# Performance work log

Hardware: AMD Instinct MI355X
Metric: run time of the kernel (lower is better)

Reference implementation:

```python
import jax, jax.numpy as jnp
import numpy as np

B, S, D, H, HD, L, V = 32, 512, 512, 8, 64, 6, 64000
EPS = 1e-5

def _layer_norm(x, g, b):
    mu = jnp.mean(x, axis=-1, keepdims=True)
    var = jnp.mean(jnp.square(x - mu), axis=-1, keepdims=True)
    return (x - mu) * jax.lax.rsqrt(var + EPS) * g + b

def _sinusoidal_pe():
    pos = np.arange(S)[:, None].astype(np.float32)
    div = np.exp(np.arange(0, D, 2).astype(np.float32) * -(np.log(10000.0) / D))
    pe = np.zeros((S, D), dtype=np.float32)
    pe[:, 0::2] = np.sin(pos * div)
    pe[:, 1::2] = np.cos(pos * div)
    return jnp.asarray(pe)

def setup_inputs() -> dict:
    key = jax.random.key(0)
    ks = jax.random.split(key, 8)
    std = 0.02
    return {
        'tokens': jax.random.randint(ks[0], (B, S), 0, V),
        'mask': jnp.ones((B, S), dtype=jnp.int32),
        'emb': jax.random.normal(ks[1], (V, D), jnp.float32) * std,
        'pe': _sinusoidal_pe(),
        'Wq': jax.random.normal(ks[2], (L, H, D, HD), jnp.float32) * std,
        'Wk': jax.random.normal(ks[3], (L, H, D, HD), jnp.float32) * std,
        'Wv': jax.random.normal(ks[4], (L, H, D, HD), jnp.float32) * std,
        'Wo': jax.random.normal(ks[5], (L, D, D), jnp.float32) * std,
        'ln1_g': jnp.ones((L, D), jnp.float32),
        'ln1_b': jnp.zeros((L, D), jnp.float32),
        'W1': jax.random.normal(ks[6], (L, D, 4 * D), jnp.float32) * std,
        'b1': jnp.zeros((L, 4 * D), jnp.float32),
        'W2': jax.random.normal(ks[7], (L, 4 * D, D), jnp.float32) * std,
        'b2': jnp.zeros((L, D), jnp.float32),
        'ln2_g': jnp.ones((L, D), jnp.float32),
        'ln2_b': jnp.zeros((L, D), jnp.float32),
    }

def reference(tokens, mask, emb, pe, Wq, Wk, Wv, Wo, ln1_g, ln1_b, W1, b1, W2, b2, ln2_g, ln2_b):
    # Eval mode: all dropouts are identity.
    x = emb[tokens] + pe[None, :S, :]               # [B,S,D]
    neg_inf = jnp.finfo(x.dtype).min
    mask_b = (mask == 0)[:, None, None, :]          # [B,1,1,S] broadcast over heads & queries
    scale = HD ** -0.5
    for l in range(L):
        q = jnp.einsum('bsd,hde->bhse', x, Wq[l])
        k = jnp.einsum('bsd,hde->bhse', x, Wk[l])
        v = jnp.einsum('bsd,hde->bhse', x, Wv[l])
        w = jnp.einsum('bhse,bhte->bhst', q, k) * scale
        w = jnp.where(mask_b, neg_inf, w)
        a = jax.nn.softmax(w, axis=-1)
        o = jnp.einsum('bhst,bhte->bhse', a, v)     # [B,H,S,HD]
        o = o.transpose(0, 2, 1, 3).reshape(x.shape[0], S, D)  # concat heads
        x = _layer_norm(x + o @ Wo[l], ln1_g[l], ln1_b[l])
        h = jax.nn.gelu(x @ W1[l] + b1[l], approximate=False) @ W2[l] + b2[l]
        x = _layer_norm(x + h, ln2_g[l], ln2_b[l])
    return x
```

## Files before the change

### kernel.cpp

```cpp
#include <hip/hip_runtime.h>

#define BB 32
#define SS 512
#define DD 512
#define HH 8
#define HDH 64
#define LL 6
#define DFF 2048
#define MM (BB*SS)

typedef __attribute__((ext_vector_type(4))) float f32x4;
typedef __attribute__((ext_vector_type(8))) short s16x8;
typedef __attribute__((ext_vector_type(4))) short s16x4;

__device__ __forceinline__ unsigned short f2bf(float f) {
    union { float f; unsigned u; } v; v.f = f;
    unsigned r = v.u + 0x7fffu + ((v.u >> 16) & 1u);
    return (unsigned short)(r >> 16);
}
__device__ __forceinline__ float bf2f(unsigned short b) {
    union { unsigned u; float f; } v; v.u = ((unsigned)b) << 16;
    return v.f;
}

__device__ __forceinline__ f32x4 mfma_bf16(s16x8 a, s16x8 b, f32x4 c) {
    asm("v_mfma_f32_16x16x32_bf16 %0, %1, %2, %0" : "+v"(c) : "v"(a), "v"(b));
    return c;
}

__device__ __forceinline__ void gload_lds16(const void* g, void* l) {
    __builtin_amdgcn_global_load_lds(
        (__attribute__((address_space(1))) void*)g,
        (__attribute__((address_space(3))) void*)l, 16, 0, 0);
}

__device__ __forceinline__ void tile_transpose_conv(
    const float* __restrict__ src, int srcPitch,
    unsigned short* __restrict__ dst, int dstPitch,
    float* lt)
{
    const int t = threadIdx.x;
    #pragma unroll
    for (int it = 0; it < 4; ++it) {
        int r = it * 16 + (t >> 4);
        int c = (t & 15) * 4;
        f32x4 v = *(const f32x4*)(src + (size_t)r * srcPitch + c);
        lt[r * 65 + c + 0] = v[0];
        lt[r * 65 + c + 1] = v[1];
        lt[r * 65 + c + 2] = v[2];
        lt[r * 65 + c + 3] = v[3];
    }
    __syncthreads();
    int nn = t >> 2;
    int kc = (t & 3) * 16;
    s16x8 o0, o1;
    #pragma unroll
    for (int i = 0; i < 8; ++i)  o0[i] = (short)f2bf(lt[(kc + i) * 65 + nn]);
    #pragma unroll
    for (int i = 0; i < 8; ++i)  o1[i] = (short)f2bf(lt[(kc + 8 + i) * 65 + nn]);
    *(s16x8*)(dst + (size_t)nn * dstPitch + kc) = o0;
    *(s16x8*)(dst + (size_t)nn * dstPitch + kc + 8) = o1;
}

__global__ __launch_bounds__(256) void k_tconv_qkv(const float* __restrict__ Wq,
                                                   const float* __restrict__ Wk,
                                                   const float* __restrict__ Wv,
                                                   unsigned short* __restrict__ dst) {
    __shared__ float lt[64 * 65];
    int bid = blockIdx.x;
    int which = bid / 384;
    int rem = bid - which * 384;
    int l = rem >> 6;
    int h = (rem >> 3) & 7;
    int kt = rem & 7;
    const float* W = which == 0 ? Wq : (which == 1 ? Wk : Wv);
    const float* srcT = W + (((size_t)(l * HH + h) * 512) + kt * 64) * 64;
    unsigned short* dstT = dst + ((size_t)l * 1536 + which * 512 + h * 64) * 512 + kt * 64;
    tile_transpose_conv(srcT, 64, dstT, 512, lt);
}

__global__ __launch_bounds__(256) void k_tconv_w(const float* __restrict__ src,
                                                 unsigned short* __restrict__ dst,
                                                 int K, int N) {
    __shared__ float lt[64 * 65];
    int tpb = (K >> 6) * (N >> 6);
    int bid = blockIdx.x;
    int l = bid / tpb;
    int rem = bid - l * tpb;
    int kt = rem / (N >> 6);
    int ntile = rem - kt * (N >> 6);
    const float* srcT = src + (size_t)l * K * N + (size_t)(kt * 64) * N + ntile * 64;
    unsigned short* dstT = dst + (size_t)l * N * K + (size_t)(ntile * 64) * K + kt * 64;
    tile_transpose_conv(srcT, N, dstT, K, lt);
}

__global__ __launch_bounds__(256) void k_embed(const int* __restrict__ tokens,
                                               const float* __restrict__ emb,
                                               const float* __restrict__ pe,
                                               float* __restrict__ x,
                                               unsigned short* __restrict__ xh) {
    int i = blockIdx.x * 256 + threadIdx.x;
    int row = i >> 7;
    int d4 = (i & 127) * 4;
    int srow = row & (SS - 1);
    int tok = tokens[row];
    f32x4 ev = *(const f32x4*)(emb + (size_t)tok*DD + d4);
    f32x4 pv = *(const f32x4*)(pe + (size_t)srow*DD + d4);
    f32x4 vv; s16x4 hv;
    #pragma unroll
    for (int j = 0; j < 4; ++j) {
        vv[j] = ev[j] + pv[j];
        hv[j] = (short)f2bf(vv[j]);
    }
    *(f32x4*)(x + (size_t)row*DD + d4) = vv;
    *(s16x4*)(xh + (size_t)row*DD + d4) = hv;
}

__global__ __launch_bounds__(128) void k_ln(const float* __restrict__ x,
                                            const float* __restrict__ y,
                                            const float* __restrict__ gg,
                                            const float* __restrict__ bb,
                                            float* __restrict__ xo,
                                            unsigned short* __restrict__ xh) {
    const int row = blockIdx.x;
    const int tid = threadIdx.x;
    __shared__ float red[4];
    f32x4 xv = *(const f32x4*)(x + (size_t)row*DD + tid*4);
    f32x4 yv = *(const f32x4*)(y + (size_t)row*DD + tid*4);
    f32x4 vv;
    #pragma unroll
    for (int j = 0; j < 4; ++j) vv[j] = xv[j] + yv[j];
    float sum = vv[0] + vv[1] + vv[2] + vv[3];
    #pragma unroll
    for (int off = 1; off < 64; off <<= 1) sum += __shfl_xor(sum, off);
    if ((tid & 63) == 0) red[tid >> 6] = sum;
    __syncthreads();
    float mu = (red[0] + red[1]) * (1.0f / 512.0f);
    float s2 = 0.0f;
    #pragma unroll
    for (int j = 0; j < 4; ++j) { float d = vv[j] - mu; s2 += d * d; }
    #pragma unroll
    for (int off = 1; off < 64; off <<= 1) s2 += __shfl_xor(s2, off);
    if ((tid & 63) == 0) red[2 + (tid >> 6)] = s2;
    __syncthreads();
    float var = (red[2] + red[3]) * (1.0f / 512.0f);
    float rs = rsqrtf(var + 1e-5f);
    f32x4 gv = *(const f32x4*)(gg + tid*4);
    f32x4 bv = *(const f32x4*)(bb + tid*4);
    f32x4 ov; s16x4 hv;
    #pragma unroll
    for (int j = 0; j < 4; ++j) {
        float o = (vv[j] - mu) * rs * gv[j] + bv[j];
        ov[j] = o;
        hv[j] = (short)f2bf(o);
    }
    *(f32x4*)(xo + (size_t)row*DD + tid*4) = ov;
    *(s16x4*)(xh + (size_t)row*DD + tid*4) = hv;
}

template<int EPI>
__global__ __launch_bounds__(256, 2) void k_gemm(
    const unsigned short* __restrict__ A, const unsigned short* __restrict__ Bt,
    unsigned short* __restrict__ ob, float* __restrict__ of,
    const float* __restrict__ bias, int N, int K, int nt)
{
    __shared__ short lds[2][2][4096];
    const int tid = threadIdx.x;
    const int lane = tid & 63;
    const int wid = tid >> 6;
    const int g = lane >> 4;
    const int t16 = lane & 15;

    int nwg = gridDim.x;
    int bid = blockIdx.x;
    int cpx = nwg >> 3;
    int swz = (bid & 7) * cpx + (bid >> 3);
    int bm = swz / nt;
    int bn = swz - bm * nt;

    const unsigned short* Ag = A  + (size_t)bm * 128 * K;
    const unsigned short* Bg = Bt + (size_t)bn * 128 * K;

    auto stage = [&](int buf, int k0) {
        #pragma unroll
        for (int i = 0; i < 2; ++i) {
            int slot = i * 256 + tid;
            int r = slot >> 2;
            int j = slot & 3;
            int js = j ^ ((r >> 1) & 3);
            size_t go = (size_t)r * K + k0 + js * 8;
            int lo = i * 2048 + wid * 512;
            gload_lds16(Ag + go, &lds[buf][0][lo]);
            gload_lds16(Bg + go, &lds[buf][1][lo]);
        }
    };

    f32x4 acc[4][4];
    #pragma unroll
    for (int a_ = 0; a_ < 4; ++a_)
        #pragma unroll
        for (int b_ = 0; b_ < 4; ++b_) acc[a_][b_] = (f32x4){0.f, 0.f, 0.f, 0.f};

    const int wm = wid >> 1, wn = wid & 1;
    stage(0, 0);
    __syncthreads();
    int nk = K >> 5;
    int buf = 0;
    for (int kt = 0; kt < nk; ++kt) {
        if (kt + 1 < nk) stage(buf ^ 1, (kt + 1) << 5);
        s16x8 af[4], bf_[4];
        #pragma unroll
        for (int mt = 0; mt < 4; ++mt) {
            int r = wm * 64 + mt * 16 + t16;
            af[mt] = *(const s16x8*)&lds[buf][0][r * 32 + ((g ^ ((r >> 1) & 3)) << 3)];
        }
        #pragma unroll
        for (int nt_ = 0; nt_ < 4; ++nt_) {
            int r = wn * 64 + nt_ * 16 + t16;
            bf_[nt_] = *(const s16x8*)&lds[buf][1][r * 32 + ((g ^ ((r >> 1) & 3)) << 3)];
        }
        #pragma unroll
        for (int mt = 0; mt < 4; ++mt)
            #pragma unroll
            for (int nt_ = 0; nt_ < 4; ++nt_)
                acc[mt][nt_] = mfma_bf16(af[mt], bf_[nt_], acc[mt][nt_]);
        __syncthreads();
        buf ^= 1;
    }

    #pragma unroll
    for (int mt = 0; mt < 4; ++mt)
        #pragma unroll
        for (int nt_ = 0; nt_ < 4; ++nt_) {
            int row0 = bm * 128 + wm * 64 + mt * 16 + g * 4;
            int col  = bn * 128 + wn * 64 + nt_ * 16 + t16;
            f32x4 v = acc[mt][nt_];
            float bv = (EPI == 2 || EPI == 3) ? bias[col] : 0.0f;
            #pragma unroll
            for (int r_ = 0; r_ < 4; ++r_) {
                size_t idx = (size_t)(row0 + r_) * N + col;
                if (EPI == 0) {
                    ob[idx] = f2bf(v[r_]);
                } else if (EPI == 1) {
                    of[idx] = v[r_];
                } else if (EPI == 2) {
                    float tv = v[r_] + bv;
                    float ge = 0.5f * tv * (1.0f + erff(tv * 0.70710678118f));
                    ob[idx] = f2bf(ge);
                } else {
                    of[idx] = v[r_] + bv;
                }
            }
        }
}

__global__ __launch_bounds__(1024, 4) void k_attn(
    const unsigned short* __restrict__ qkv, const int* __restrict__ mask,
    unsigned short* __restrict__ o)
{
    extern __shared__ short smem[];
    short* Kl = smem;
    short* Vl = smem + 32768;
    const int tid = threadIdx.x;
    const int lane = tid & 63, wid = tid >> 6;
    short* Pl = smem + 65536 + wid * 1024;
    const int b = blockIdx.x >> 3, h = blockIdx.x & 7;
    const unsigned short* base = qkv + (size_t)b * SS * 1536;
    const int qc = h * 64, kc = 512 + h * 64, vc = 1024 + h * 64;

    for (int c = tid; c < 4096; c += 1024) {
        int t = c >> 3, j = c & 7;
        s16x8 kv = *(const s16x8*)(base + (size_t)t * 1536 + kc + j * 8);
        *(s16x8*)(Kl + t * 64 + ((j ^ (t & 7)) << 3)) = kv;
    }
    {
        int unit = tid >> 1, half = tid & 1;
        int t0 = (unit >> 3) << 3, e0 = (unit & 7) << 3;
        s16x8 r0 = *(const s16x8*)(base + (size_t)(t0 + half*4 + 0) * 1536 + vc + e0);
        s16x8 r1 = *(const s16x8*)(base + (size_t)(t0 + half*4 + 1) * 1536 + vc + e0);
        s16x8 r2 = *(const s16x8*)(base + (size_t)(t0 + half*4 + 2) * 1536 + vc + e0);
        s16x8 r3 = *(const s16x8*)(base + (size_t)(t0 + half*4 + 3) * 1536 + vc + e0);
        #pragma unroll
        for (int j = 0; j < 8; ++j) {
            int e = e0 + j;
            int slot = (t0 >> 3) ^ (e & 7) ^ ((e >> 3) & 7);
            s16x4 w = (s16x4){r0[j], r1[j], r2[j], r3[j]};
            *(s16x4*)(Vl + e * 512 + (slot << 3) + (half << 2)) = w;
        }
    }
    const int g = lane >> 4, t16 = lane & 15;
    unsigned mbits = 0;
    for (int n2 = 0; n2 < 32; ++n2)
        if (mask[b * SS + n2 * 16 + t16] != 0) mbits |= (1u << n2);
    __syncthreads();

    for (int qi = 0; qi < 2; ++qi) {
        const int q0 = (wid * 2 + qi) * 16;
        s16x8 aq[2];
        #pragma unroll
        for (int ks = 0; ks < 2; ++ks)
            aq[ks] = *(const s16x8*)(base + (size_t)(q0 + t16) * 1536 + qc + ks * 32 + g * 8);

        f32x4 oacc[4];
        #pragma unroll
        for (int eo = 0; eo < 4; ++eo) oacc[eo] = (f32x4){0.f, 0.f, 0.f, 0.f};
        float mx[4] = {-3.0e38f, -3.0e38f, -3.0e38f, -3.0e38f};
        float ls[4] = {0.f, 0.f, 0.f, 0.f};

        for (int tc = 0; tc < 4; ++tc) {
            f32x4 s[8];
            #pragma unroll
            for (int n2 = 0; n2 < 8; ++n2) s[n2] = (f32x4){0.f, 0.f, 0.f, 0.f};
            #pragma unroll
            for (int n2 = 0; n2 < 8; ++n2) {
                int t = tc * 128 + n2 * 16 + t16;
                #pragma unroll
                for (int ks = 0; ks < 2; ++ks) {
                    int blk = ks * 4 + g;
                    s16x8 bk = *(const s16x8*)(Kl + t * 64 + ((blk ^ (t & 7)) << 3));
                    s[n2] = mfma_bf16(aq[ks], bk, s[n2]);
                }
            }
            #pragma unroll
            for (int n2 = 0; n2 < 8; ++n2) {
                bool val = (mbits >> (tc * 8 + n2)) & 1u;
                #pragma unroll
                for (int r_ = 0; r_ < 4; ++r_)
                    s[n2][r_] = val ? s[n2][r_] * 0.125f : -3.0e38f;
            }
            float sc[4];
            #pragma unroll
            for (int r_ = 0; r_ < 4; ++r_) {
                float m = s[0][r_];
                #pragma unroll
                for (int n2 = 1; n2 < 8; ++n2) m = fmaxf(m, s[n2][r_]);
                #pragma unroll
                for (int off = 1; off < 16; off <<= 1) m = fmaxf(m, __shfl_xor(m, off));
                float mn = fmaxf(mx[r_], m);
                sc[r_] = __expf(mx[r_] - mn);
                mx[r_] = mn;
                ls[r_] *= sc[r_];
            }
            #pragma unroll
            for (int eo = 0; eo < 4; ++eo)
                #pragma unroll
                for (int r_ = 0; r_ < 4; ++r_) oacc[eo][r_] *= sc[r_];
            #pragma unroll
            for (int n2 = 0; n2 < 8; ++n2)
                #pragma unroll
                for (int r_ = 0; r_ < 4; ++r_)
                    s[n2][r_] = __expf(s[n2][r_] - mx[r_]);
            #pragma unroll
            for (int r_ = 0; r_ < 4; ++r_) {
                float t = 0.f;
                #pragma unroll
                for (int n2 = 0; n2 < 8; ++n2) t += s[n2][r_];
                #pragma unroll
                for (int off = 1; off < 16; off <<= 1) t += __shfl_xor(t, off);
                ls[r_] += t;
            }
            #pragma unroll
            for (int c4 = 0; c4 < 2; ++c4) {
                #pragma unroll
                for (int k4 = 0; k4 < 4; ++k4) {
                    int n2 = c4 * 4 + k4;
                    #pragma unroll
                    for (int r_ = 0; r_ < 4; ++r_) {
                        int qq = g * 4 + r_;
                        int kk = k4 * 16 + t16;
                        Pl[qq * 64 + (((kk >> 3) ^ (qq & 7)) << 3) + (kk & 7)] =
                            (short)f2bf(s[n2][r_]);
                    }
                }
                #pragma unroll
                for (int ks2 = 0; ks2 < 2; ++ks2) {
                    int kk = ks2 * 32 + g * 8;
                    s16x8 pa = *(const s16x8*)(Pl + t16 * 64 + (((kk >> 3) ^ (t16 & 7)) << 3));
                    int tg = tc * 128 + c4 * 64 + kk;
                    #pragma unroll
                    for (int eo = 0; eo < 4; ++eo) {
                        int e = eo * 16 + t16;
                        int slot = (tg >> 3) ^ (e & 7) ^ ((e >> 3) & 7);
                        s16x8 bv = *(const s16x8*)(Vl + e * 512 + (slot << 3));
                        oacc[eo] = mfma_bf16(pa, bv, oacc[eo]);
                    }
                }
            }
        }
        #pragma unroll
        for (int eo = 0; eo < 4; ++eo)
            #pragma unroll
            for (int r_ = 0; r_ < 4; ++r_) {
                int row = q0 + g * 4 + r_;
                int e = eo * 16 + t16;
                o[((size_t)b * SS + row) * DD + h * HDH + e] =
                    f2bf(oacc[eo][r_] / ls[r_]);
            }
    }
}

extern "C" void kernel_launch(void* const* d_in, const int* in_sizes, int n_in,
                              void* d_out, int out_size, void* d_ws, size_t ws_size,
                              hipStream_t stream)
{
    const int*   tokens = (const int*)d_in[0];
    const int*   mask   = (const int*)d_in[1];
    const float* emb    = (const float*)d_in[2];
    const float* pe     = (const float*)d_in[3];
    const float* Wq     = (const float*)d_in[4];
    const float* Wk     = (const float*)d_in[5];
    const float* Wv     = (const float*)d_in[6];
    const float* Wo     = (const float*)d_in[7];
    const float* l1g    = (const float*)d_in[8];
    const float* l1b    = (const float*)d_in[9];
    const float* W1     = (const float*)d_in[10];
    const float* b1     = (const float*)d_in[11];
    const float* W2     = (const float*)d_in[12];
    const float* b2     = (const float*)d_in[13];
    const float* l2g    = (const float*)d_in[14];
    const float* l2b    = (const float*)d_in[15];

    char* p = (char*)d_ws;
    auto alloc = [&](size_t bytes) { char* r = p; p += (bytes + 255) & ~(size_t)255; return r; };
    unsigned short* wqkv_t = (unsigned short*)alloc((size_t)LL*3*DD*DD*2);
    unsigned short* wo_t   = (unsigned short*)alloc((size_t)LL*DD*DD*2);
    unsigned short* w1_t   = (unsigned short*)alloc((size_t)LL*DD*DFF*2);
    unsigned short* w2_t   = (unsigned short*)alloc((size_t)LL*DD*DFF*2);
    float*          x      = (float*)alloc((size_t)MM*DD*4);
    unsigned short* xh     = (unsigned short*)alloc((size_t)MM*DD*2);
    unsigned short* qkvb   = (unsigned short*)alloc((size_t)MM*1536*2);
    unsigned short* obuf   = (unsigned short*)alloc((size_t)MM*DD*2);
    float*          ybuf   = (float*)alloc((size_t)MM*DD*4);
    unsigned short* hbuf   = qkvb;

    k_tconv_qkv<<<1152, 256, 0, stream>>>(Wq, Wk, Wv, wqkv_t);
    k_tconv_w<<<384, 256, 0, stream>>>(Wo, wo_t, 512, 512);
    k_tconv_w<<<1536, 256, 0, stream>>>(W1, w1_t, 512, 2048);
    k_tconv_w<<<1536, 256, 0, stream>>>(W2, w2_t, 2048, 512);
    k_embed<<<8192, 256, 0, stream>>>(tokens, emb, pe, x, xh);

    hipFuncSetAttribute((const void*)k_attn,
                        hipFuncAttributeMaxDynamicSharedMemorySize, 163840);

    for (int l = 0; l < LL; ++l) {
        const unsigned short* wqkvl = wqkv_t + (size_t)l*3*DD*DD;
        const unsigned short* wol   = wo_t   + (size_t)l*DD*DD;
        const unsigned short* w1l   = w1_t   + (size_t)l*DD*DFF;
        const unsigned short* w2l   = w2_t   + (size_t)l*DD*DFF;

        k_gemm<0><<<1536, 256, 0, stream>>>(xh, wqkvl, qkvb, nullptr, nullptr, 1536, 512, 12);
        k_attn<<<256, 1024, 163840, stream>>>(qkvb, mask, obuf);
        k_gemm<1><<<512, 256, 0, stream>>>(obuf, wol, nullptr, ybuf, nullptr, 512, 512, 4);
        k_ln<<<16384, 128, 0, stream>>>(x, ybuf, l1g + l*DD, l1b + l*DD, x, xh);
        k_gemm<2><<<2048, 256, 0, stream>>>(xh, w1l, hbuf, nullptr, b1 + (size_t)l*DFF, 2048, 512, 16);
        k_gemm<3><<<512, 256, 0, stream>>>(hbuf, w2l, nullptr, ybuf, b2 + (size_t)l*DD, 512, 2048, 4);
        float* xout = (l == LL - 1) ? (float*)d_out : x;
        k_ln<<<16384, 128, 0, stream>>>(x, ybuf, l2g + l*DD, l2b + l*DD, xout, xh);
    }
}
```

Before: 1.442 ms.

## Add 256x128 triple-buffered GEMM for W2 and store residual branch in bf16

Result: faster. 1.383 ms (-4.1%).

```diff
diff --git a/kernel.cpp b/kernel.cpp
--- a/kernel.cpp
+++ b/kernel.cpp
@@ -117,7 +117,7 @@
 }
 
 __global__ __launch_bounds__(128) void k_ln(const float* __restrict__ x,
-                                            const float* __restrict__ y,
+                                            const unsigned short* __restrict__ y,
                                             const float* __restrict__ gg,
                                             const float* __restrict__ bb,
                                             float* __restrict__ xo,
@@ -126,10 +126,10 @@
     const int tid = threadIdx.x;
     __shared__ float red[4];
     f32x4 xv = *(const f32x4*)(x + (size_t)row*DD + tid*4);
-    f32x4 yv = *(const f32x4*)(y + (size_t)row*DD + tid*4);
+    s16x4 yv = *(const s16x4*)(y + (size_t)row*DD + tid*4);
     f32x4 vv;
     #pragma unroll
-    for (int j = 0; j < 4; ++j) vv[j] = xv[j] + yv[j];
+    for (int j = 0; j < 4; ++j) vv[j] = xv[j] + bf2f((unsigned short)yv[j]);
     float sum = vv[0] + vv[1] + vv[2] + vv[3];
     #pragma unroll
     for (int off = 1; off < 64; off <<= 1) sum += __shfl_xor(sum, off);
@@ -161,7 +161,7 @@
 template<int EPI>
 __global__ __launch_bounds__(256, 2) void k_gemm(
     const unsigned short* __restrict__ A, const unsigned short* __restrict__ Bt,
-    unsigned short* __restrict__ ob, float* __restrict__ of,
+    unsigned short* __restrict__ ob,
     const float* __restrict__ bias, int N, int K, int nt)
 {
     __shared__ short lds[2][2][4096];
@@ -235,22 +235,144 @@
             int row0 = bm * 128 + wm * 64 + mt * 16 + g * 4;
             int col  = bn * 128 + wn * 64 + nt_ * 16 + t16;
             f32x4 v = acc[mt][nt_];
-            float bv = (EPI == 2 || EPI == 3) ? bias[col] : 0.0f;
+            float bv = (EPI == 2) ? bias[col] : 0.0f;
             #pragma unroll
             for (int r_ = 0; r_ < 4; ++r_) {
                 size_t idx = (size_t)(row0 + r_) * N + col;
                 if (EPI == 0) {
                     ob[idx] = f2bf(v[r_]);
-                } else if (EPI == 1) {
-                    of[idx] = v[r_];
-                } else if (EPI == 2) {
+                } else {
                     float tv = v[r_] + bv;
                     float ge = 0.5f * tv * (1.0f + erff(tv * 0.70710678118f));
                     ob[idx] = f2bf(ge);
-                } else {
-                    of[idx] = v[r_] + bv;
                 }
             }
+        }
+}
+
+__global__ __launch_bounds__(512, 2) void k_gemm8(
+    const unsigned short* __restrict__ A, const unsigned short* __restrict__ Bt,
+    unsigned short* __restrict__ ob,
+    const float* __restrict__ bias, int N, int K, int nt)
+{
+    extern __shared__ short lds[];
+    const int tid = threadIdx.x;
+    const int lane = tid & 63;
+    const int wid = tid >> 6;
+    const int g = lane >> 4;
+    const int t16 = lane & 15;
+    const int wm = wid >> 2, wn = wid & 3;
+
+    int nwg = gridDim.x;
+    int bid = blockIdx.x;
+    int cpx = nwg >> 3;
+    int swz = (bid & 7) * cpx + (bid >> 3);
+    int bm = swz / nt;
+    int bn = swz - bm * nt;
+
+    const unsigned short* Ag = A  + (size_t)bm * 256 * K;
+    const unsigned short* Bg = Bt + (size_t)bn * 128 * K;
+
+    auto stage_unit = [&](int slot, int t, int unit) {
+        const int k0 = t << 6;
+        const unsigned short* src = (unit == 2) ? Bg : (Ag + (unit ? (size_t)128 * K : 0));
+        short* dst0 = lds + slot * 24576 + (unit == 2 ? 16384 : unit * 8192);
+        #pragma unroll
+        for (int rr = 0; rr < 2; ++rr) {
+            int rb = rr * 64 + wid * 8;
+            int r_in = rb + (lane >> 3);
+            int c = (lane & 7) ^ (r_in & 7);
+            gload_lds16(src + (size_t)r_in * K + k0 + c * 8, dst0 + rb * 64);
+        }
+    };
+
+    f32x4 acc[8][2];
+    #pragma unroll
+    for (int a_ = 0; a_ < 8; ++a_)
+        #pragma unroll
+        for (int b_ = 0; b_ < 2; ++b_) acc[a_][b_] = (f32x4){0.f, 0.f, 0.f, 0.f};
+
+    const int nk = K >> 6;
+    stage_unit(0, 0, 0); stage_unit(0, 0, 1); stage_unit(0, 0, 2);
+    stage_unit(1, 1, 0); stage_unit(1, 1, 1); stage_unit(1, 1, 2);
+
+    int slot = 0;
+    for (int t = 0; t < nk; ++t) {
+        if (t + 1 < nk) asm volatile("s_waitcnt vmcnt(6)" ::: "memory");
+        else            asm volatile("s_waitcnt vmcnt(0)" ::: "memory");
+        __builtin_amdgcn_s_barrier();
+        __builtin_amdgcn_sched_barrier(0);
+
+        int s2 = slot + 2; if (s2 >= 3) s2 -= 3;
+        const short* As = lds + slot * 24576;
+        const short* Bs = As + 16384;
+
+        if (t + 2 < nk) { stage_unit(s2, t + 2, 0); stage_unit(s2, t + 2, 1); }
+        s16x8 bfr[2][2];
+        #pragma unroll
+        for (int nn = 0; nn < 2; ++nn) {
+            int row = wn * 32 + nn * 16 + t16;
+            #pragma unroll
+            for (int kk = 0; kk < 2; ++kk)
+                bfr[nn][kk] = *(const s16x8*)&Bs[row * 64 + (((kk * 4 + g) ^ (row & 7)) << 3)];
+        }
+        {
+            s16x8 afr[4][2];
+            #pragma unroll
+            for (int mm = 0; mm < 4; ++mm) {
+                int row = wm * 128 + mm * 16 + t16;
+                #pragma unroll
+                for (int kk = 0; kk < 2; ++kk)
+                    afr[mm][kk] = *(const s16x8*)&As[row * 64 + (((kk * 4 + g) ^ (row & 7)) << 3)];
+            }
+            __builtin_amdgcn_sched_barrier(0);
+            __builtin_amdgcn_s_setprio(1);
+            #pragma unroll
+            for (int mm = 0; mm < 4; ++mm)
+                #pragma unroll
+                for (int nn = 0; nn < 2; ++nn)
+                    #pragma unroll
+                    for (int kk = 0; kk < 2; ++kk)
+                        acc[mm][nn] = mfma_bf16(afr[mm][kk], bfr[nn][kk], acc[mm][nn]);
+            __builtin_amdgcn_s_setprio(0);
+            __builtin_amdgcn_sched_barrier(0);
+        }
+        if (t + 2 < nk) stage_unit(s2, t + 2, 2);
+        {
+            s16x8 afr[4][2];
+            #pragma unroll
+            for (int mm = 0; mm < 4; ++mm) {
+                int row = wm * 128 + (mm + 4) * 16 + t16;
+                #pragma unroll
+                for (int kk = 0; kk < 2; ++kk)
+                    afr[mm][kk] = *(const s16x8*)&As[row * 64 + (((kk * 4 + g) ^ (row & 7)) << 3)];
+            }
+            __builtin_amdgcn_sched_barrier(0);
+            __builtin_amdgcn_s_setprio(1);
+            #pragma unroll
+            for (int mm = 0; mm < 4; ++mm)
+                #pragma unroll
+                for (int nn = 0; nn < 2; ++nn)
+                    #pragma unroll
+                    for (int kk = 0; kk < 2; ++kk)
+                        acc[mm + 4][nn] = mfma_bf16(afr[mm][kk], bfr[nn][kk], acc[mm + 4][nn]);
+            __builtin_amdgcn_s_setprio(0);
+            __builtin_amdgcn_sched_barrier(0);
+        }
+        slot = slot + 1 == 3 ? 0 : slot + 1;
+    }
+
+    #pragma unroll
+    for (int mm = 0; mm < 8; ++mm)
+        #pragma unroll
+        for (int nn = 0; nn < 2; ++nn) {
+            int row0 = bm * 256 + wm * 128 + mm * 16 + g * 4;
+            int col  = bn * 128 + wn * 32 + nn * 16 + t16;
+            f32x4 v = acc[mm][nn];
+            float bv = bias[col];
+            #pragma unroll
+            for (int r_ = 0; r_ < 4; ++r_)
+                ob[(size_t)(row0 + r_) * N + col] = f2bf(v[r_] + bv);
         }
 }
 
@@ -430,7 +552,7 @@
     unsigned short* xh     = (unsigned short*)alloc((size_t)MM*DD*2);
     unsigned short* qkvb   = (unsigned short*)alloc((size_t)MM*1536*2);
     unsigned short* obuf   = (unsigned short*)alloc((size_t)MM*DD*2);
-    float*          ybuf   = (float*)alloc((size_t)MM*DD*4);
+    unsigned short* ybufb  = (unsigned short*)alloc((size_t)MM*DD*2);
     unsigned short* hbuf   = qkvb;
 
     k_tconv_qkv<<<1152, 256, 0, stream>>>(Wq, Wk, Wv, wqkv_t);
@@ -441,6 +563,8 @@
 
     hipFuncSetAttribute((const void*)k_attn,
                         hipFuncAttributeMaxDynamicSharedMemorySize, 163840);
+    hipFuncSetAttribute((const void*)k_gemm8,
+                        hipFuncAttributeMaxDynamicSharedMemorySize, 147456);
 
     for (int l = 0; l < LL; ++l) {
         const unsigned short* wqkvl = wqkv_t + (size_t)l*3*DD*DD;
@@ -448,13 +572,13 @@
         const unsigned short* w1l   = w1_t   + (size_t)l*DD*DFF;
         const unsigned short* w2l   = w2_t   + (size_t)l*DD*DFF;
 
-        k_gemm<0><<<1536, 256, 0, stream>>>(xh, wqkvl, qkvb, nullptr, nullptr, 1536, 512, 12);
+        k_gemm<0><<<1536, 256, 0, stream>>>(xh, wqkvl, qkvb, nullptr, 1536, 512, 12);
         k_attn<<<256, 1024, 163840, stream>>>(qkvb, mask, obuf);
-        k_gemm<1><<<512, 256, 0, stream>>>(obuf, wol, nullptr, ybuf, nullptr, 512, 512, 4);
-        k_ln<<<16384, 128, 0, stream>>>(x, ybuf, l1g + l*DD, l1b + l*DD, x, xh);
-        k_gemm<2><<<2048, 256, 0, stream>>>(xh, w1l, hbuf, nullptr, b1 + (size_t)l*DFF, 2048, 512, 16);
-        k_gemm<3><<<512, 256, 0, stream>>>(hbuf, w2l, nullptr, ybuf, b2 + (size_t)l*DD, 512, 2048, 4);
+        k_gemm<0><<<512, 256, 0, stream>>>(obuf, wol, ybufb, nullptr, 512, 512, 4);
+        k_ln<<<16384, 128, 0, stream>>>(x, ybufb, l1g + l*DD, l1b + l*DD, x, xh);
+        k_gemm<2><<<2048, 256, 0, stream>>>(xh, w1l, hbuf, b1 + (size_t)l*DFF, 2048, 512, 16);
+        k_gemm8<<<256, 512, 147456, stream>>>(hbuf, w2l, ybufb, b2 + (size_t)l*DD, 512, 2048, 4);
         float* xout = (l == LL - 1) ? (float*)d_out : x;
-        k_ln<<<16384, 128, 0, stream>>>(x, ybuf, l2g + l*DD, l2b + l*DD, xout, xh);
-    }
-}
+        k_ln<<<16384, 128, 0, stream>>>(x, ybufb, l2g + l*DD, l2b + l*DD, xout, xh);
+    }
+}
```
